# Kernel tuning notes

Hardware: AMD Instinct MI355X
Metric: run time of the kernel (lower is better)

The kernel has to match this reference:

```python
import jax, jax.numpy as jnp
import numpy as np

B, NCLASS, NSUPP = 4096, 1000, 64
NCHUNK = NSUPP * NSUPP  # 4096, x's feature dim


def setup_inputs() -> dict:
    key = jax.random.key(0)
    k1, k2, k3 = jax.random.split(key, 3)
    x = jax.random.normal(k1, (B, NCHUNK), dtype=jnp.float32)
    # torch .uniform_(-1, 1)
    wSupp = jax.random.uniform(k2, (NCLASS, NSUPP), dtype=jnp.float32, minval=-1.0, maxval=1.0)
    chunk_map = jax.random.randint(k3, (NCLASS, NSUPP), 0, NCHUNK, dtype=jnp.int32)
    return {"x": x, "wSupp": wSupp, "chunk_map": chunk_map}


def reference(x, wSupp, chunk_map):
    # sparse_support: for each class i, feat_i = sum_j x[:, chunk_map[i,j]] * wSupp[i,j]; out = exp(feat)
    gathered = x[:, chunk_map]                      # [B, nClass, nSupp] gather via index map
    feats = jnp.einsum('bcs,cs->bc', gathered, wSupp)  # weighted sum over support
    return jnp.exp(feats)                           # [B, nClass]
```

## Files before the change

### kernel.cpp

```cpp
#include <hip/hip_runtime.h>
#include <hip/hip_fp16.h>


constexpr int B_       = 4096;
constexpr int NCLASS_  = 1000;
constexpr int NSUPP_   = 64;
constexpr int NCHUNK_  = 4096;
constexpr int BT       = 16;
constexpr int THREADS_ = 1024;
constexpr int SG_      = NSUPP_ / 4;
constexpr size_t CMT_BYTES = (size_t)SG_ * NCLASS_ * 16;
constexpr size_t WS_NEEDED = 2 * CMT_BYTES;

__global__ __launch_bounds__(256)
void build_cw_kernel(const int*   __restrict__ cm,
                     const float* __restrict__ w,
                     int*         __restrict__ cmT,
                     float*       __restrict__ wT)
{
    const int t    = threadIdx.x;
    const int c    = blockIdx.x * 4 + (t >> 6);
    const int lane = t & 63;
    if (c >= NCLASS_) return;

    const int   idx = cm[c * NSUPP_ + lane];
    const float wv  = w [c * NSUPP_ + lane];
    const int   key = (idx - c) & 3;

    const unsigned long long below = ((unsigned long long)1 << lane) - 1;
    int j = 0;
    #pragma unroll
    for (int r = 0; r < 4; ++r) {
        const unsigned long long m = __ballot(key == r);
        if (key > r)  j += __popcll(m);
        if (key == r) j += __popcll(m & below);
    }

    const int dst = ((j >> 2) * NCLASS_ + c) * 4 + (j & 3);
    cmT[dst] = idx;
    wT [dst] = wv;
}

template <bool USET>
__global__ __launch_bounds__(THREADS_, 4)
void supp_gather_kernel(const float* __restrict__ x,
                        const float* __restrict__ wSupp,
                        const int*   __restrict__ cmap,
                        const float4* __restrict__ wT,
                        const int4*   __restrict__ cmT,
                        float*       __restrict__ out)
{
    __shared__ __align__(16) __half2 tile[NCHUNK_ * (BT / 2)];

    const int t  = threadIdx.x;
    const int rb = blockIdx.x * BT;

    int4   ci;
    float4 wf;
    if (t < NCLASS_) {
        if constexpr (USET) { ci = cmT[t]; wf = wT[t]; }
        else {
            ci = reinterpret_cast<const int4*>(cmap + t * NSUPP_)[0];
            wf = reinterpret_cast<const float4*>(wSupp + t * NSUPP_)[0];
        }
    }

    #pragma unroll
    for (int p = 0; p < NCHUNK_ / THREADS_; ++p) {
        const int col = t + THREADS_ * p;
        float v[BT];
        #pragma unroll
        for (int bi = 0; bi < BT; ++bi)
            v[bi] = x[(size_t)(rb + bi) * NCHUNK_ + col];
        __half2 h[BT / 2];
        #pragma unroll
        for (int k = 0; k < BT / 2; ++k)
            h[k] = __floats2half2_rn(v[2 * k], v[2 * k + 1]);
        *reinterpret_cast<float4*>(&tile[(size_t)col * 8]) =
            *reinterpret_cast<float4*>(&h[0]);
        *reinterpret_cast<float4*>(&tile[(size_t)col * 8 + 4]) =
            *reinterpret_cast<float4*>(&h[4]);
    }
    __syncthreads();

    if (t < NCLASS_) {
        const int c = t;
        const float4* tile4 = reinterpret_cast<const float4*>(tile);
        float acc[BT];
        #pragma unroll
        for (int bi = 0; bi < BT; ++bi) acc[bi] = 0.f;

        for (int sg = 0; sg < SG_; ++sg) {
            float4 d0a = tile4[2 * ci.x],     d0b = tile4[2 * ci.x + 1];
            float4 d1a = tile4[2 * ci.y],     d1b = tile4[2 * ci.y + 1];
            float4 d2a = tile4[2 * ci.z],     d2b = tile4[2 * ci.z + 1];
            float4 d3a = tile4[2 * ci.w],     d3b = tile4[2 * ci.w + 1];
            const float4 wv = wf;

            const int sgn = (sg + 1 < SG_) ? sg + 1 : SG_ - 1;
            if constexpr (USET) {
                ci = cmT[sgn * NCLASS_ + c];
                wf = wT [sgn * NCLASS_ + c];
            } else {
                ci = reinterpret_cast<const int4*>(cmap + c * NSUPP_)[sgn];
                wf = reinterpret_cast<const float4*>(wSupp + c * NSUPP_)[sgn];
            }

            const float4* dpa[4] = {&d0a, &d1a, &d2a, &d3a};
            const float4* dpb[4] = {&d0b, &d1b, &d2b, &d3b};
            const float   ws4[4] = {wv.x, wv.y, wv.z, wv.w};
            #pragma unroll
            for (int j = 0; j < 4; ++j) {
                const __half2* ha = reinterpret_cast<const __half2*>(dpa[j]);
                const __half2* hb = reinterpret_cast<const __half2*>(dpb[j]);
                #pragma unroll
                for (int k = 0; k < 4; ++k) {
                    const float2 fa = __half22float2(ha[k]);
                    const float2 fb = __half22float2(hb[k]);
                    acc[2 * k]      = fmaf(fa.x, ws4[j], acc[2 * k]);
                    acc[2 * k + 1]  = fmaf(fa.y, ws4[j], acc[2 * k + 1]);
                    acc[8 + 2 * k]     = fmaf(fb.x, ws4[j], acc[8 + 2 * k]);
                    acc[8 + 2 * k + 1] = fmaf(fb.y, ws4[j], acc[8 + 2 * k + 1]);
                }
            }
        }
        #pragma unroll
        for (int bi = 0; bi < BT; ++bi)
            out[(size_t)(rb + bi) * NCLASS_ + c] = __expf(acc[bi]);
    }
}

extern "C" void kernel_launch(void* const* d_in, const int* in_sizes, int n_in,
                              void* d_out, int out_size, void* d_ws, size_t ws_size,
                              hipStream_t stream) {
    const float* x  = (const float*)d_in[0];
    const float* w  = (const float*)d_in[1];
    const int*   cm = (const int*)d_in[2];
    float*       o  = (float*)d_out;

    int*   cmT = (int*)d_ws;
    float* wT  = (float*)((char*)d_ws + CMT_BYTES);

    const dim3 grid(B_ / BT);
    if (ws_size >= WS_NEEDED) {
        build_cw_kernel<<<dim3((NCLASS_ + 3) / 4), dim3(256), 0, stream>>>(
            cm, w, cmT, wT);
        supp_gather_kernel<true><<<grid, dim3(THREADS_), 0, stream>>>(
            x, w, cm, (const float4*)wT, (const int4*)cmT, o);
    } else {
        supp_gather_kernel<false><<<grid, dim3(THREADS_), 0, stream>>>(
            x, w, cm, (const float4*)wT, (const int4*)cmT, o);
    }
}
```

Before: 116.4 us.

## Split batch tile into halves and overlap second-half loads with first-half gather

The 16-row tile is split into two 8-row halves stored in separate shared-memory regions, each holding a float4 of halves per column. Global loads for the second half are issued into registers before the first-half gather runs, so memory latency can overlap with the LDS gather compute. The gather then reads one float4 per index instead of two, and the index-permutation key in the build kernel now uses eight bank groups instead of four to reduce LDS bank conflicts. The cost is higher register pressure from holding 32 floats in flight, an extra sync, and reloading index and weight data for the second pass.

```diff
diff --git a/kernel.cpp b/kernel.cpp
--- a/kernel.cpp
+++ b/kernel.cpp
@@ -7,6 +7,7 @@
 constexpr int NSUPP_   = 64;
 constexpr int NCHUNK_  = 4096;
 constexpr int BT       = 16;
+constexpr int BH       = BT / 2;
 constexpr int THREADS_ = 1024;
 constexpr int SG_      = NSUPP_ / 4;
 constexpr size_t CMT_BYTES = (size_t)SG_ * NCLASS_ * 16;
@@ -25,12 +26,12 @@
 
     const int   idx = cm[c * NSUPP_ + lane];
     const float wv  = w [c * NSUPP_ + lane];
-    const int   key = (idx - c) & 3;
+    const int   key = (idx - c) & 7;
 
-    const unsigned long long below = ((unsigned long long)1 << lane) - 1;
+    const unsigned long long below = ((unsigned long long)1 << lane) - 1ull;
     int j = 0;
     #pragma unroll
-    for (int r = 0; r < 4; ++r) {
+    for (int r = 0; r < 8; ++r) {
         const unsigned long long m = __ballot(key == r);
         if (key > r)  j += __popcll(m);
         if (key == r) j += __popcll(m & below);
@@ -42,6 +43,41 @@
 }
 
 template <bool USET>
+__device__ __forceinline__ void gather_half(
+    const float4* __restrict__ t4,
+    const float4* __restrict__ wT, const int4* __restrict__ cmT,
+    const float* __restrict__ wSupp, const int* __restrict__ cmap,
+    const int c, int4& ci, float4& wf, float acc[BH])
+{
+    for (int sg = 0; sg < SG_; ++sg) {
+        float4 d0 = t4[ci.x], d1 = t4[ci.y], d2 = t4[ci.z], d3 = t4[ci.w];
+        const float4 wv = wf;
+
+        const int sgn = (sg + 1 < SG_) ? sg + 1 : SG_ - 1;
+        if constexpr (USET) {
+            ci = cmT[sgn * NCLASS_ + c];
+            wf = wT [sgn * NCLASS_ + c];
+        } else {
+            ci = reinterpret_cast<const int4*>(cmap + c * NSUPP_)[sgn];
+            wf = reinterpret_cast<const float4*>(wSupp + c * NSUPP_)[sgn];
+        }
+
+        const float4* dp[4]  = {&d0, &d1, &d2, &d3};
+        const float   ws4[4] = {wv.x, wv.y, wv.z, wv.w};
+        #pragma unroll
+        for (int j = 0; j < 4; ++j) {
+            const __half2* h = reinterpret_cast<const __half2*>(dp[j]);
+            #pragma unroll
+            for (int k = 0; k < 4; ++k) {
+                const float2 f = __half22float2(h[k]);
+                acc[2 * k]     = fmaf(f.x, ws4[j], acc[2 * k]);
+                acc[2 * k + 1] = fmaf(f.y, ws4[j], acc[2 * k + 1]);
+            }
+        }
+    }
+}
+
+template <bool USET>
 __global__ __launch_bounds__(THREADS_, 4)
 void supp_gather_kernel(const float* __restrict__ x,
                         const float* __restrict__ wSupp,
@@ -50,7 +86,9 @@
                         const int4*   __restrict__ cmT,
                         float*       __restrict__ out)
 {
-    __shared__ __align__(16) __half2 tile[NCHUNK_ * (BT / 2)];
+    __shared__ __align__(16) __half2 tile[NCHUNK_ * 8];
+    __half2* tlo = tile;
+    __half2* thi = tile + NCHUNK_ * 4;
 
     const int t  = threadIdx.x;
     const int rb = blockIdx.x * BT;
@@ -68,65 +106,71 @@
     #pragma unroll
     for (int p = 0; p < NCHUNK_ / THREADS_; ++p) {
         const int col = t + THREADS_ * p;
-        float v[BT];
+        float v[BH];
         #pragma unroll
-        for (int bi = 0; bi < BT; ++bi)
+        for (int bi = 0; bi < BH; ++bi)
             v[bi] = x[(size_t)(rb + bi) * NCHUNK_ + col];
-        __half2 h[BT / 2];
+        __half2 h[BH / 2];
         #pragma unroll
-        for (int k = 0; k < BT / 2; ++k)
+        for (int k = 0; k < BH / 2; ++k)
             h[k] = __floats2half2_rn(v[2 * k], v[2 * k + 1]);
-        *reinterpret_cast<float4*>(&tile[(size_t)col * 8]) =
-            *reinterpret_cast<float4*>(&h[0]);
-        *reinterpret_cast<float4*>(&tile[(size_t)col * 8 + 4]) =
-            *reinterpret_cast<float4*>(&h[4]);
+        *reinterpret_cast<float4*>(&tlo[(size_t)col * 4]) =
+            *reinterpret_cast<const float4*>(&h[0]);
+    }
+    __syncthreads();
+
+    float hv[4 * BH];
+    #pragma unroll
+    for (int p = 0; p < NCHUNK_ / THREADS_; ++p) {
+        const int col = t + THREADS_ * p;
+        #pragma unroll
+        for (int bi = 0; bi < BH; ++bi)
+            hv[p * BH + bi] = x[(size_t)(rb + BH + bi) * NCHUNK_ + col];
+    }
+    __builtin_amdgcn_sched_barrier(0);
+
+    float accl[BH];
+    if (t < NCLASS_) {
+        #pragma unroll
+        for (int bi = 0; bi < BH; ++bi) accl[bi] = 0.f;
+        gather_half<USET>(reinterpret_cast<const float4*>(tlo),
+                          wT, cmT, wSupp, cmap, t, ci, wf, accl);
+    }
+
+    #pragma unroll
+    for (int p = 0; p < NCHUNK_ / THREADS_; ++p) {
+        const int col = t + THREADS_ * p;
+        __half2 h[BH / 2];
+        #pragma unroll
+        for (int k = 0; k < BH / 2; ++k)
+            h[k] = __floats2half2_rn(hv[p * BH + 2 * k], hv[p * BH + 2 * k + 1]);
+        *reinterpret_cast<float4*>(&thi[(size_t)col * 4]) =
+            *reinterpret_cast<const float4*>(&h[0]);
+    }
+    if (t < NCLASS_) {
+        if constexpr (USET) { ci = cmT[t]; wf = wT[t]; }
+        else {
+            ci = reinterpret_cast<const int4*>(cmap + t * NSUPP_)[0];
+            wf = reinterpret_cast<const float4*>(wSupp + t * NSUPP_)[0];
+        }
     }
     __syncthreads();
 
     if (t < NCLASS_) {
         const int c = t;
-        const float4* tile4 = reinterpret_cast<const float4*>(tile);
-        float acc[BT];
         #pragma unroll
-        for (int bi = 0; bi < BT; ++bi) acc[bi] = 0.f;
+        for (int bi = 0; bi < BH; ++bi)
+            out[(size_t)(rb + bi) * NCLASS_ + c] = __expf(accl[bi]);
 
-        for (int sg = 0; sg < SG_; ++sg) {
-            float4 d0a = tile4[2 * ci.x],     d0b = tile4[2 * ci.x + 1];
-            float4 d1a = tile4[2 * ci.y],     d1b = tile4[2 * ci.y + 1];
-            float4 d2a = tile4[2 * ci.z],     d2b = tile4[2 * ci.z + 1];
-            float4 d3a = tile4[2 * ci.w],     d3b = tile4[2 * ci.w + 1];
-            const float4 wv = wf;
+        float acch[BH];
+        #pragma unroll
+        for (int bi = 0; bi < BH; ++bi) acch[bi] = 0.f;
+        gather_half<USET>(reinterpret_cast<const float4*>(thi),
+                          wT, cmT, wSupp, cmap, c, ci, wf, acch);
 
-            const int sgn = (sg + 1 < SG_) ? sg + 1 : SG_ - 1;
-            if constexpr (USET) {
-                ci = cmT[sgn * NCLASS_ + c];
-                wf = wT [sgn * NCLASS_ + c];
-            } else {
-                ci = reinterpret_cast<const int4*>(cmap + c * NSUPP_)[sgn];
-                wf = reinterpret_cast<const float4*>(wSupp + c * NSUPP_)[sgn];
-            }
-
-            const float4* dpa[4] = {&d0a, &d1a, &d2a, &d3a};
-            const float4* dpb[4] = {&d0b, &d1b, &d2b, &d3b};
-            const float   ws4[4] = {wv.x, wv.y, wv.z, wv.w};
-            #pragma unroll
-            for (int j = 0; j < 4; ++j) {
-                const __half2* ha = reinterpret_cast<const __half2*>(dpa[j]);
-                const __half2* hb = reinterpret_cast<const __half2*>(dpb[j]);
-                #pragma unroll
-                for (int k = 0; k < 4; ++k) {
-                    const float2 fa = __half22float2(ha[k]);
-                    const float2 fb = __half22float2(hb[k]);
-                    acc[2 * k]      = fmaf(fa.x, ws4[j], acc[2 * k]);
-                    acc[2 * k + 1]  = fmaf(fa.y, ws4[j], acc[2 * k + 1]);
-                    acc[8 + 2 * k]     = fmaf(fb.x, ws4[j], acc[8 + 2 * k]);
-                    acc[8 + 2 * k + 1] = fmaf(fb.y, ws4[j], acc[8 + 2 * k + 1]);
-                }
-            }
-        }
         #pragma unroll
-        for (int bi = 0; bi < BT; ++bi)
-            out[(size_t)(rb + bi) * NCLASS_ + c] = __expf(acc[bi]);
+        for (int bi = 0; bi < BH; ++bi)
+            out[(size_t)(rb + BH + bi) * NCLASS_ + c] = __expf(acch[bi]);
     }
 }
 
```

After: 116.3 us. No clear change (-0.1%).
